# Kernel tuning notes

Measured on AMD Instinct MI355X. Metric: run time of the kernel, lower is better.

Reference implementation:

```python
import jax, jax.numpy as jnp
import numpy as np
import math

B, S, H, NH, R = 1, 1024, 4096, 32, 16
HD = H // NH
BLOCK = 64
PRUNE_RATIO = 0.5
NF4_TABLE = jnp.array([
    -1.0, -0.6961928009986877, -0.5250730514526367, -0.39491748809814453,
    -0.28444138169288635, -0.18477343022823334, -0.09105003625154495, 0.0,
    0.07958029955625534, 0.16093020141124725, 0.24611230194568634,
    0.33791524171829224, 0.4407098591327667, 0.5626170039176941,
    0.7229568362236023, 1.0], dtype=jnp.float32)


def dequant_nf4(codes, absmax):
    # codes: [out,in] int4 values in [0,16); absmax: per-64-elem block scale
    vals = NF4_TABLE[codes.reshape(-1)]                 # [out*in]
    vals = vals.reshape(-1, BLOCK) * absmax[:, None]    # blockwise rescale
    return vals.reshape(codes.shape)                    # [out,in]


def setup_inputs() -> dict:
    key = jax.random.key(0)
    ks = jax.random.split(key, 32)
    d = {"x": jax.random.normal(ks[0], (B, S, H), dtype=jnp.float32)}
    i = 1
    for n in ("q", "k", "v", "o"):
        d[f"w_{n}_codes"] = jax.random.randint(ks[i], (H, H), 0, 16, dtype=jnp.int32); i += 1
        d[f"w_{n}_absmax"] = jax.random.uniform(ks[i], (H * H // BLOCK,), dtype=jnp.float32) * 0.06; i += 1
        d[f"b_{n}"] = jax.random.normal(ks[i], (H,), dtype=jnp.float32) * 0.01; i += 1
        d[f"w_{n}_lora_a"] = jax.random.normal(ks[i], (H, R), dtype=jnp.float32) * (1.0 / math.sqrt(H)); i += 1
        d[f"w_{n}_lora_b"] = jax.random.normal(ks[i], (R, H), dtype=jnp.float32) * 0.02; i += 1
    causal = jnp.tril(jnp.ones((S, S), dtype=bool))
    d["attention_mask"] = jnp.where(causal, 0.0, -1e9).astype(jnp.float32)[None, None]
    return d


def _proj(x, codes, absmax, b, la, lb):
    w = dequant_nf4(codes, absmax).T          # [in,out]
    main = x @ w + b
    lora_a = x @ la                            # [B,S,R]
    return main + lora_a @ lb, main, lora_a


def _kth_val(t, use_abs=True):
    flat = jnp.abs(t).ravel() if use_abs else t.ravel()
    k = int(t.size * PRUNE_RATIO)
    return jnp.sort(flat)[k - 1]


def reference(x, w_q_codes, w_q_absmax, b_q, w_q_lora_a, w_q_lora_b,
              w_k_codes, w_k_absmax, b_k, w_k_lora_a, w_k_lora_b,
              w_v_codes, w_v_absmax, b_v, w_v_lora_a, w_v_lora_b,
              w_o_codes, w_o_absmax, b_o, w_o_lora_a, w_o_lora_b,
              attention_mask):
    q, _, _ = _proj(x, w_q_codes, w_q_absmax, b_q, w_q_lora_a, w_q_lora_b)
    k, _, _ = _proj(x, w_k_codes, w_k_absmax, b_k, w_k_lora_a, w_k_lora_b)
    v, _, _ = _proj(x, w_v_codes, w_v_absmax, b_v, w_v_lora_a, w_v_lora_b)
    # [B,S,H] -> [B,NH,S,HD]
    qh = q.reshape(B, S, NH, HD).transpose(0, 2, 1, 3)
    kh = k.reshape(B, S, NH, HD).transpose(0, 2, 1, 3)
    vh = v.reshape(B, S, NH, HD).transpose(0, 2, 1, 3)
    s = jnp.einsum("bhqd,bhkd->bhqk", qh, kh) / math.sqrt(HD) + attention_mask
    a = jax.nn.softmax(s, axis=-1)
    o = jnp.einsum("bhqk,bhkd->bhqd", a, vh)
    o = o.transpose(0, 2, 1, 3).reshape(B, S, H)
    o_final, _, _ = _proj(o, w_o_codes, w_o_absmax, b_o, w_o_lora_a, w_o_lora_b)
    # iteration < 10 branch: magnitude-pruning thresholds via kth smallest value
    kth_vals = jnp.stack([
        _kth_val(x), _kth_val(qh), _kth_val(kh), _kth_val(vh),
        _kth_val(a, use_abs=False), _kth_val(o)])
    return o_final, kth_vals
```

## Files before the change

### kernel.cpp

```cpp
#include <hip/hip_runtime.h>

#define S_LEN  1024
#define H_DIM  4096
#define NHEAD  32
#define HEAD_D 128
#define RANK   16
#define KE3    4160
#define KEO    4160
#define TOTP   ((long)NHEAD * S_LEN * S_LEN)

typedef __bf16 bf16x8 __attribute__((ext_vector_type(8)));
typedef float  f32x4  __attribute__((ext_vector_type(4)));
typedef unsigned short ushort8v __attribute__((ext_vector_type(8)));

#define GLOAD_LDS16(g, l) __builtin_amdgcn_global_load_lds( \
    (const __attribute__((address_space(1))) unsigned int*)(g), \
    (__attribute__((address_space(3))) unsigned int*)(l), 16, 0, 0)

__device__ const float NF4_TAB[16] = {
    -1.0f, -0.6961928009986877f, -0.5250730514526367f, -0.39491748809814453f,
    -0.28444138169288635f, -0.18477343022823334f, -0.09105003625154495f, 0.0f,
    0.07958029955625534f, 0.16093020141124725f, 0.24611230194568634f,
    0.33791524171829224f, 0.4407098591327667f, 0.5626170039176941f,
    0.7229568362236023f, 1.0f};

__device__ __forceinline__ unsigned short f2bf(float f) {
    unsigned int u = __builtin_bit_cast(unsigned int, f);
    u = (u + 0x7FFFu + ((u >> 16) & 1u)) >> 16;
    return (unsigned short)u;
}

__device__ __forceinline__ float bf2f(unsigned short s) {
    return __builtin_bit_cast(float, (unsigned int)s << 16);
}

__device__ __forceinline__ void dequant_body(
    const int* __restrict__ codes, const float* __restrict__ absmax,
    unsigned short* __restrict__ out, long i, int ostride) {
    int4 c0 = *(const int4*)(codes + i);
    int4 c1 = *(const int4*)(codes + i + 4);
    float am = absmax[i >> 6];
    long orow = i >> 12;
    int  col  = (int)(i & 4095);
    ushort8v r;
    r[0] = f2bf(NF4_TAB[c0.x] * am);
    r[1] = f2bf(NF4_TAB[c0.y] * am);
    r[2] = f2bf(NF4_TAB[c0.z] * am);
    r[3] = f2bf(NF4_TAB[c0.w] * am);
    r[4] = f2bf(NF4_TAB[c1.x] * am);
    r[5] = f2bf(NF4_TAB[c1.y] * am);
    r[6] = f2bf(NF4_TAB[c1.z] * am);
    r[7] = f2bf(NF4_TAB[c1.w] * am);
    *(ushort8v*)(out + orow * ostride + col) = r;
}

__global__ __launch_bounds__(256) void xcast_lora(
    const float* __restrict__ x, const float* __restrict__ la0,
    const float* __restrict__ la1, const float* __restrict__ la2,
    unsigned short* __restrict__ xb_ext) {
    __shared__ float xs[4096];
    int m = (int)blockIdx.x;
    int tid = threadIdx.x;
    const float* xr = x + (long)m * H_DIM;
    int c = tid * 16;
    float4 f0 = *(const float4*)(xr + c);
    float4 f1 = *(const float4*)(xr + c + 4);
    float4 f2 = *(const float4*)(xr + c + 8);
    float4 f3 = *(const float4*)(xr + c + 12);
    *(float4*)(xs + c)      = f0;
    *(float4*)(xs + c + 4)  = f1;
    *(float4*)(xs + c + 8)  = f2;
    *(float4*)(xs + c + 12) = f3;
    ushort8v r0, r1;
    r0[0] = f2bf(f0.x); r0[1] = f2bf(f0.y); r0[2] = f2bf(f0.z); r0[3] = f2bf(f0.w);
    r0[4] = f2bf(f1.x); r0[5] = f2bf(f1.y); r0[6] = f2bf(f1.z); r0[7] = f2bf(f1.w);
    r1[0] = f2bf(f2.x); r1[1] = f2bf(f2.y); r1[2] = f2bf(f2.z); r1[3] = f2bf(f2.w);
    r1[4] = f2bf(f3.x); r1[5] = f2bf(f3.y); r1[6] = f2bf(f3.z); r1[7] = f2bf(f3.w);
    unsigned short* orow = xb_ext + (long)m * KE3 + c;
    *(ushort8v*)orow = r0;
    *(ushort8v*)(orow + 8) = r1;
    __syncthreads();
    int w = tid >> 6, lane = tid & 63;
    if (w < 3) {
        const float* la = (w == 0) ? la0 : (w == 1) ? la1 : la2;
        float s[16];
#pragma unroll
        for (int r = 0; r < 16; ++r) s[r] = 0.f;
        for (int k = lane; k < H_DIM; k += 64) {
            float xv = xs[k];
            const float4* lr = (const float4*)(la + (long)k * RANK);
            float4 q0 = lr[0], q1 = lr[1], q2 = lr[2], q3 = lr[3];
            s[0] += xv * q0.x;  s[1] += xv * q0.y;  s[2] += xv * q0.z;  s[3] += xv * q0.w;
            s[4] += xv * q1.x;  s[5] += xv * q1.y;  s[6] += xv * q1.z;  s[7] += xv * q1.w;
            s[8] += xv * q2.x;  s[9] += xv * q2.y;  s[10] += xv * q2.z; s[11] += xv * q2.w;
            s[12] += xv * q3.x; s[13] += xv * q3.y; s[14] += xv * q3.z; s[15] += xv * q3.w;
        }
        for (int off = 32; off; off >>= 1)
#pragma unroll
            for (int r = 0; r < 16; ++r) s[r] += __shfl_xor(s[r], off);
        if (lane == 0)
#pragma unroll
            for (int r = 0; r < 16; ++r)
                xb_ext[(long)m * KE3 + 4096 + 16 * w + r] = f2bf(s[r]);
    } else if (lane < 16) {
        xb_ext[(long)m * KE3 + 4144 + lane] = 0;
    }
}

__global__ __launch_bounds__(256) void prep_weights(
    const int* __restrict__ c0, const int* __restrict__ c1,
    const int* __restrict__ c2, const int* __restrict__ c3,
    const float* __restrict__ a0, const float* __restrict__ a1,
    const float* __restrict__ a2, const float* __restrict__ a3,
    const float* __restrict__ lb0, const float* __restrict__ lb1,
    const float* __restrict__ lb2, const float* __restrict__ lb3,
    const float* __restrict__ b0, const float* __restrict__ b1,
    const float* __restrict__ b2,
    unsigned short* __restrict__ wqkv, unsigned short* __restrict__ wo,
    float* __restrict__ bias3, unsigned int* __restrict__ hist, long n) {
    int p = blockIdx.y;
    long bx = blockIdx.x;
    int tid = threadIdx.x;
    if (bx < 8192) {
        const int* codes = (p == 0) ? c0 : (p == 1) ? c1 : (p == 2) ? c2 : c3;
        const float* am  = (p == 0) ? a0 : (p == 1) ? a1 : (p == 2) ? a2 : a3;
        long i = (bx * 256 + tid) * 8;
        if (i >= n) return;
        if (p < 3) dequant_body(codes, am, wqkv + (size_t)p * H_DIM * KE3, i, KE3);
        else       dequant_body(codes, am, wo, i, KEO);
        return;
    }
    if (bx < 9216) {
        long g = (bx - 8192) * 256 + tid;
        int row = (int)(g >> 6), c = (int)(g & 63);
        if (p < 3) {
            const float* lb = (p == 0) ? lb0 : (p == 1) ? lb1 : lb2;
            unsigned int r = (unsigned int)(c - 16 * p);
            float v = (r < 16u) ? lb[r * H_DIM + row] : 0.f;
            wqkv[(size_t)p * H_DIM * KE3 + (long)row * KE3 + 4096 + c] = f2bf(v);
            if (g < H_DIM) {
                const float* bp = (p == 0) ? b0 : (p == 1) ? b1 : b2;
                bias3[(size_t)p * H_DIM + g] = bp[g];
            }
            return;
        }
        float v = (c < 16) ? lb3[c * H_DIM + row] : 0.f;
        wo[(long)row * KEO + 4096 + c] = f2bf(v);
        return;
    }
    if (p == 1) {
        long g = (bx - 9216) * 256 + tid;
        if (g < 6 * 16384) hist[g] = 0u;
    }
}

__global__ __launch_bounds__(256) void lora_ao_kernel(
    unsigned short* __restrict__ ob_ext, const float* __restrict__ la) {
    int m = blockIdx.x;
    const unsigned short* xr = ob_ext + (long)m * KEO;
    int tid = threadIdx.x, lane = tid & 63, wid = tid >> 6;
    float s[4] = {0.f, 0.f, 0.f, 0.f};
    for (int k0 = lane * 8; k0 < H_DIM; k0 += 512) {
        ushort8v xv8 = *(const ushort8v*)(xr + k0);
#pragma unroll
        for (int j = 0; j < 8; ++j) {
            float xv = bf2f(xv8[j]);
            float4 q = *(const float4*)(la + (long)(k0 + j) * RANK + wid * 4);
            s[0] += xv * q.x; s[1] += xv * q.y;
            s[2] += xv * q.z; s[3] += xv * q.w;
        }
    }
    for (int off = 32; off; off >>= 1)
        for (int r = 0; r < 4; ++r) s[r] += __shfl_down(s[r], off);
    if (lane == 0) {
        for (int r = 0; r < 4; ++r)
            ob_ext[(long)m * KEO + 4096 + wid * 4 + r] = f2bf(s[r]);
        for (int r = 0; r < 12; ++r)
            ob_ext[(long)m * KEO + 4112 + wid * 12 + r] = 0;
    }
}

template<int MODE>
__global__ __launch_bounds__(256) void gemm_nt(
    const unsigned short* __restrict__ A, const unsigned short* __restrict__ B,
    void* __restrict__ Cv, void* __restrict__ Cv2, const float* __restrict__ bias,
    int K, int lda, int ldb, int ldc,
    long strideA, long strideB, long strideC, float alpha,
    const unsigned short* __restrict__ tsrc, unsigned short* __restrict__ tdst) {
    __shared__ unsigned short As[128][64];
    __shared__ unsigned short Bs[128][64];
    const int tid = threadIdx.x;
    int bm, bn;
    int k0s = 0, k0e = K;
    if (MODE == 1) {
        int i = blockIdx.x;
        if (i >= 36) {
            unsigned short (*tl)[33] = (unsigned short(*)[33])&As[0][0];
            int tb = (i - 36) + 4 * blockIdx.z;
            int tx = tid & 31, ty = tid >> 5;
            for (int tile = tb; tile < 4096; tile += 128) {
                int tc = tile & 127, ts = tile >> 7;
                int c0 = tc * 32, s0 = ts * 32;
                for (int j = 0; j < 32; j += 8)
                    tl[ty + j][tx] = tsrc[(long)(s0 + ty + j) * H_DIM + c0 + tx];
                __syncthreads();
                for (int j = 0; j < 32; j += 8)
                    tdst[(long)(c0 + ty + j) * S_LEN + s0 + tx] = tl[tx][ty + j];
                __syncthreads();
            }
            return;
        }
        int tm = (int)((sqrtf(8.f * i + 1.f) - 1.f) * 0.5f);
        if ((tm + 1) * (tm + 2) / 2 <= i) tm++;
        if (tm * (tm + 1) / 2 > i) tm--;
        int tn = i - tm * (tm + 1) / 2;
        bm = tm * 128; bn = tn * 128;
    } else {
        bm = blockIdx.y * 128; bn = blockIdx.x * 128;
        if (MODE == 2) { int kl = bm + 128; if (kl < k0e) k0e = kl; }
    }
    const unsigned short* Ab = A;
    const unsigned short* Bb = B;
    long coff = 0;
    void* Cuse = Cv;
    if (MODE == 3) {
        int Kh = (K / 2) & ~63;
        k0s = blockIdx.z ? Kh : 0;
        k0e = blockIdx.z ? K : Kh;
        Cuse = blockIdx.z ? Cv2 : Cv;
    } else {
        Ab += (long)blockIdx.z * strideA;
        Bb += (long)blockIdx.z * strideB;
        coff = (long)blockIdx.z * strideC;
    }
    const int lane = tid & 63, wid = tid >> 6;
    const int wm = (wid >> 1) * 64, wn = (wid & 1) * 64;
    const int srow = lane >> 3;
    const int scol = ((lane & 7) ^ srow) << 3;
    const int r0 = wid * 8 + srow;
    const unsigned short* gA0 = Ab + (long)(bm + r0) * lda + scol;
    const unsigned short* gB0 = Bb + (long)(bn + r0) * ldb + scol;
    f32x4 acc[4][4] = {};
    const int q = lane >> 4, rr = lane & 15;
    const int colh0 = ((q ^ (rr & 7)) << 3);
    const int colh1 = colh0 ^ 32;
    for (int k0 = k0s; k0 < k0e; k0 += 64) {
#pragma unroll
        for (int p = 0; p < 4; ++p) {
            GLOAD_LDS16(gA0 + (long)p * 32 * lda + k0, &As[p * 32 + wid * 8][0]);
            GLOAD_LDS16(gB0 + (long)p * 32 * ldb + k0, &Bs[p * 32 + wid * 8][0]);
        }
        __syncthreads();
        bf16x8 af[4], bfr[4];
#pragma unroll
        for (int i = 0; i < 4; ++i) {
            af[i]  = __builtin_bit_cast(bf16x8, *(const uint4*)&As[wm + i * 16 + rr][colh0]);
            bfr[i] = __builtin_bit_cast(bf16x8, *(const uint4*)&Bs[wn + i * 16 + rr][colh0]);
        }
#pragma unroll
        for (int i = 0; i < 4; ++i)
#pragma unroll
            for (int j = 0; j < 4; ++j)
                acc[i][j] = __builtin_amdgcn_mfma_f32_16x16x32_bf16(
                    af[i], bfr[j], acc[i][j], 0, 0, 0);
#pragma unroll
        for (int i = 0; i < 4; ++i) {
            af[i]  = __builtin_bit_cast(bf16x8, *(const uint4*)&As[wm + i * 16 + rr][colh1]);
            bfr[i] = __builtin_bit_cast(bf16x8, *(const uint4*)&Bs[wn + i * 16 + rr][colh1]);
        }
#pragma unroll
        for (int i = 0; i < 4; ++i)
#pragma unroll
            for (int j = 0; j < 4; ++j)
                acc[i][j] = __builtin_amdgcn_mfma_f32_16x16x32_bf16(
                    af[i], bfr[j], acc[i][j], 0, 0, 0);
        __syncthreads();
    }
    const int cr = (lane >> 4) * 4;
    const int cc = lane & 15;
    float bv[4];
#pragma unroll
    for (int j = 0; j < 4; ++j)
        bv[j] = bias ? bias[(long)blockIdx.z * H_DIM + bn + wn + j * 16 + cc] : 0.f;
    if (MODE != 3) {
        unsigned short* Cb = (unsigned short*)Cuse + coff;
        for (int i = 0; i < 4; ++i)
            for (int j = 0; j < 4; ++j) {
                unsigned short* cp = Cb + (long)(bm + wm + i * 16 + cr) * ldc
                                        + (bn + wn + j * 16 + cc);
                for (int r = 0; r < 4; ++r)
                    cp[(long)r * ldc] = f2bf(acc[i][j][r] * alpha + bv[j]);
            }
    } else {
        float* Cb = (float*)Cuse + coff;
        for (int i = 0; i < 4; ++i)
            for (int j = 0; j < 4; ++j) {
                float* cp = Cb + (long)(bm + wm + i * 16 + cr) * ldc
                               + (bn + wn + j * 16 + cc);
                for (int r = 0; r < 4; ++r)
                    cp[(long)r * ldc] = acc[i][j][r] * alpha + bv[j];
            }
    }
}

__global__ __launch_bounds__(256) void softmax_causal(unsigned short* __restrict__ scores16) {
    int b = blockIdx.x;
    int h = b >> 9, pr = b & 511;
    int tid = threadIdx.x, lane = tid & 63, wid = tid >> 6;
    __shared__ float red[4], red2[4];
    for (int half = 0; half < 2; ++half) {
        int i = half ? (S_LEN - 1 - pr) : pr;
        unsigned short* row = scores16 + ((long)h * S_LEN + i) * S_LEN;
        int L = i + 1;
        float v[4];
        float mx = -1e30f;
        for (int t = 0; t < 4; ++t) {
            int j = tid + (t << 8);
            v[t] = (j < L) ? bf2f(row[j]) : -1e30f;
            mx = fmaxf(mx, v[t]);
        }
        for (int off = 32; off; off >>= 1) mx = fmaxf(mx, __shfl_xor(mx, off));
        if (lane == 0) red[wid] = mx;
        __syncthreads();
        mx = fmaxf(fmaxf(red[0], red[1]), fmaxf(red[2], red[3]));
        float e[4], sum = 0.f;
        for (int t = 0; t < 4; ++t) {
            int j = tid + (t << 8);
            e[t] = (j < L) ? __expf(v[t] - mx) : 0.f;
            sum += e[t];
        }
        for (int off = 32; off; off >>= 1) sum += __shfl_xor(sum, off);
        if (lane == 0) red2[wid] = sum;
        __syncthreads();
        sum = red2[0] + red2[1] + red2[2] + red2[3];
        float inv = 1.f / sum;
        for (int t = 0; t < 4; ++t) {
            int j = tid + (t << 8);
            row[j] = f2bf(e[t] * inv);
        }
        __syncthreads();
    }
}

__global__ __launch_bounds__(256, 2) void hist6(
    const float* __restrict__ x, const unsigned short* __restrict__ qkv,
    const unsigned short* __restrict__ ob, const unsigned short* __restrict__ P,
    unsigned int* __restrict__ hist) {
    __shared__ unsigned int lh[16384];
    const long SH = (long)S_LEN * H_DIM;
    int t = threadIdx.x;
    int b = blockIdx.x;
    int ten, b0, nblk;
    if (b < 256)      { ten = 0; b0 = 0;   nblk = 256; }
    else if (b < 384) { ten = 1; b0 = 256; nblk = 128; }
    else if (b < 512) { ten = 2; b0 = 384; nblk = 128; }
    else if (b < 640) { ten = 3; b0 = 512; nblk = 128; }
    else if (b < 768) { ten = 4; b0 = 640; nblk = 128; }
    else              { ten = 5; b0 = 768; nblk = 768; }
    unsigned int* gh = hist + (long)ten * 16384;
    for (int k = t; k < 16384; k += 256) lh[k] = 0u;
    __syncthreads();
    long i = (long)(b - b0) * 256 + t;
    long stride = (long)nblk * 256;
    if (ten == 0) {
        for (; i < SH / 4; i += stride) {
            float4 v = *(const float4*)(x + i * 4);
            unsigned int u0 = (__builtin_bit_cast(unsigned int, v.x) & 0x7FFFFFFFu) >> 16;
            unsigned int u1 = (__builtin_bit_cast(unsigned int, v.y) & 0x7FFFFFFFu) >> 16;
            unsigned int u2 = (__builtin_bit_cast(unsigned int, v.z) & 0x7FFFFFFFu) >> 16;
            unsigned int u3 = (__builtin_bit_cast(unsigned int, v.w) & 0x7FFFFFFFu) >> 16;
            atomicAdd(&lh[u0 < 16384u ? u0 : 16383u], 1u);
            atomicAdd(&lh[u1 < 16384u ? u1 : 16383u], 1u);
            atomicAdd(&lh[u2 < 16384u ? u2 : 16383u], 1u);
            atomicAdd(&lh[u3 < 16384u ? u3 : 16383u], 1u);
        }
    } else if (ten <= 3) {
        const unsigned short* src = qkv + (size_t)(ten - 1) * SH;
        for (; i < SH / 8; i += stride) {
            ushort8v v = ((const ushort8v*)src)[i];
#pragma unroll
            for (int j = 0; j < 8; ++j) {
                unsigned int u = v[j] & 0x7FFFu;
                atomicAdd(&lh[u < 16384u ? u : 16383u], 1u);
            }
        }
    } else if (ten == 4) {
        for (; i < SH / 8; i += stride) {
            long off = (i >> 9) * KEO + ((i & 511) << 3);
            ushort8v v = *(const ushort8v*)(ob + off);
#pragma unroll
            for (int j = 0; j < 8; ++j) {
                unsigned int u = v[j] & 0x7FFFu;
                atomicAdd(&lh[u < 16384u ? u : 16383u], 1u);
            }
        }
    } else {
        unsigned int zc = 0;
        for (; i < TOTP / 8; i += stride) {
            ushort8v v = ((const ushort8v*)P)[i];
#pragma unroll
            for (int j = 0; j < 8; ++j) {
                unsigned int bb = v[j];
                if (bb == 0) zc++;
                else atomicAdd(&lh[bb < 16384u ? bb : 16383u], 1u);
            }
        }
        if (zc) atomicAdd(&lh[0], zc);
    }
    __syncthreads();
    for (int k = t; k < 16384; k += 256) {
        unsigned int c = lh[k];
        if (c) atomicAdd(&gh[k], c);
    }
}

__global__ __launch_bounds__(256) void finish_kernel(
    float* __restrict__ out, const float* __restrict__ part,
    const float* __restrict__ bias, const unsigned int* __restrict__ hist,
    float* __restrict__ out_kth) {
    int b = blockIdx.x;
    int t = threadIdx.x;
    if (b < 4096) {
        long idx = ((long)b * 256 + t) * 4;
        int n = (int)(idx & 4095);
        float4 o = *(float4*)(out + idx);
        float4 p = *(const float4*)(part + idx);
        float4 bb = *(const float4*)(bias + n);
        o.x += p.x + bb.x; o.y += p.y + bb.y; o.z += p.z + bb.z; o.w += p.w + bb.w;
        *(float4*)(out + idx) = o;
        return;
    }
    int ten = b - 4096;
    const unsigned int* h = hist + (long)ten * 16384;
    __shared__ unsigned int partl[256];
    unsigned int s = 0;
    for (int bb = 0; bb < 64; ++bb) s += h[t * 64 + bb];
    partl[t] = s;
    __syncthreads();
    if (t == 0) {
        long k = (ten == 5) ? TOTP / 2 : (long)S_LEN * H_DIM / 2;
        long c = 0;
        int ch = 0;
        for (; ch < 256; ++ch) {
            if (c + (long)partl[ch] >= k) break;
            c += partl[ch];
        }
        int bin = ch * 64;
        for (;; ++bin) {
            unsigned int hv = h[bin];
            if (c + (long)hv >= k) break;
            c += hv;
        }
        int slot = (ten == 4) ? 5 : (ten == 5) ? 4 : ten;
        out_kth[slot] = __builtin_bit_cast(float, (unsigned int)bin << 16);
    }
}

extern "C" void kernel_launch(void* const* d_in, const int* in_sizes, int n_in,
                              void* d_out, int out_size, void* d_ws, size_t ws_size,
                              hipStream_t stream) {
    (void)in_sizes; (void)n_in; (void)out_size; (void)ws_size;
    const float* x = (const float*)d_in[0];
    const int*   wcodes[4] = {(const int*)d_in[1], (const int*)d_in[6],
                              (const int*)d_in[11], (const int*)d_in[16]};
    const float* wabs[4]   = {(const float*)d_in[2], (const float*)d_in[7],
                              (const float*)d_in[12], (const float*)d_in[17]};
    const float* bias[4]   = {(const float*)d_in[3], (const float*)d_in[8],
                              (const float*)d_in[13], (const float*)d_in[18]};
    const float* lA[4]     = {(const float*)d_in[4], (const float*)d_in[9],
                              (const float*)d_in[14], (const float*)d_in[19]};
    const float* lB[4]     = {(const float*)d_in[5], (const float*)d_in[10],
                              (const float*)d_in[15], (const float*)d_in[20]};

    char* wp = (char*)d_ws;
    auto alloc = [&](size_t bytes) {
        char* p = wp; wp += (bytes + 255) & ~(size_t)255; return p;
    };
    const size_t SH  = (size_t)S_LEN * H_DIM;
    const long   nW  = (long)H_DIM * H_DIM;
    unsigned short* xb_ext = (unsigned short*)alloc((size_t)S_LEN * KE3 * 2);
    unsigned short* qkvb   = (unsigned short*)alloc(3 * SH * 2);
    unsigned short* vT     = (unsigned short*)alloc(SH * 2);
    unsigned short* ob_ext = (unsigned short*)alloc((size_t)S_LEN * KEO * 2);
    unsigned short* Wd_ext = (unsigned short*)alloc((size_t)H_DIM * KEO * 2);
    float*        opart  = (float*)alloc(SH * 4);
    float*        bias3  = (float*)alloc(3 * H_DIM * 4);
    unsigned int* hist   = (unsigned int*)alloc(6 * 16384 * 4);
    char* bigbuf = alloc((size_t)3 * H_DIM * KE3 * 2);
    unsigned short* Wqkv_ext = (unsigned short*)bigbuf;
    unsigned short* scores16 = (unsigned short*)bigbuf;

    float* out_final = (float*)d_out;
    float* out_kth   = out_final + SH;

    unsigned short* qb = qkvb;
    unsigned short* kb = qkvb + SH;
    unsigned short* vb = qkvb + 2 * SH;

    xcast_lora<<<S_LEN, 256, 0, stream>>>(x, lA[0], lA[1], lA[2], xb_ext);

    prep_weights<<<dim3(9600, 4), 256, 0, stream>>>(
        wcodes[0], wcodes[1], wcodes[2], wcodes[3],
        wabs[0], wabs[1], wabs[2], wabs[3],
        lB[0], lB[1], lB[2], lB[3],
        bias[0], bias[1], bias[2],
        Wqkv_ext, Wd_ext, bias3, hist, nW);

    gemm_nt<0><<<dim3(32, 8, 3), 256, 0, stream>>>(
        xb_ext, Wqkv_ext, qkvb, nullptr, bias3, KE3, KE3, KE3, H_DIM,
        0, (long)H_DIM * KE3, (long)SH, 1.0f, nullptr, nullptr);

    gemm_nt<1><<<dim3(40, 1, NHEAD), 256, 0, stream>>>(
        qb, kb, scores16, nullptr, nullptr, HEAD_D, H_DIM, H_DIM, S_LEN,
        128, 128, (long)S_LEN * S_LEN, 0.08838834764831845f, vb, vT);

    softmax_causal<<<NHEAD * S_LEN / 2, 256, 0, stream>>>(scores16);

    gemm_nt<2><<<dim3(1, 8, NHEAD), 256, 0, stream>>>(
        scores16, vT, ob_ext, nullptr, nullptr, S_LEN,
        S_LEN, S_LEN, KEO,
        (long)S_LEN * S_LEN, (long)HEAD_D * S_LEN, 128, 1.0f, nullptr, nullptr);

    lora_ao_kernel<<<S_LEN, 256, 0, stream>>>(ob_ext, lA[3]);

    gemm_nt<3><<<dim3(32, 8, 2), 256, 0, stream>>>(
        ob_ext, Wd_ext, out_final, opart, nullptr, KEO, KEO, KEO, H_DIM,
        0, 0, 0, 1.0f, nullptr, nullptr);

    hist6<<<1536, 256, 0, stream>>>(x, qkvb, ob_ext, scores16, hist);

    finish_kernel<<<4102, 256, 0, stream>>>(out_final, opart, bias[3], hist, out_kth);
}
```

Measured before the change: 722.5 us.

## Overlap O-projection weight dequant with QKV GEMM via extra blocks

The O-projection NF4 dequantization moves out of prep_weights into 192 extra blocks of the QKV GEMM launch, so it runs alongside the GEMM tiles instead of before them. The O LoRA-B padding columns are now written by xcast_lora. The GEMM template becomes a device body wrapped by per-mode kernels with constant arguments. This shortens the serial prep phase, at the cost of the dequant blocks competing with GEMM tiles for CUs and memory bandwidth.

```diff
diff --git a/kernel.cpp b/kernel.cpp
--- a/kernel.cpp
+++ b/kernel.cpp
@@ -57,10 +57,17 @@
 __global__ __launch_bounds__(256) void xcast_lora(
     const float* __restrict__ x, const float* __restrict__ la0,
     const float* __restrict__ la1, const float* __restrict__ la2,
-    unsigned short* __restrict__ xb_ext) {
+    const float* __restrict__ lb3,
+    unsigned short* __restrict__ xb_ext, unsigned short* __restrict__ wo) {
     __shared__ float xs[4096];
     int m = (int)blockIdx.x;
     int tid = threadIdx.x;
+    {
+        long g = (long)m * 256 + tid;
+        int row = (int)(g >> 6), c = (int)(g & 63);
+        float v = (c < 16) ? lb3[c * H_DIM + row] : 0.f;
+        wo[(long)row * KEO + 4096 + c] = f2bf(v);
+    }
     const float* xr = x + (long)m * H_DIM;
     int c = tid * 16;
     float4 f0 = *(const float4*)(xr + c);
@@ -109,43 +116,37 @@
 
 __global__ __launch_bounds__(256) void prep_weights(
     const int* __restrict__ c0, const int* __restrict__ c1,
-    const int* __restrict__ c2, const int* __restrict__ c3,
+    const int* __restrict__ c2,
     const float* __restrict__ a0, const float* __restrict__ a1,
-    const float* __restrict__ a2, const float* __restrict__ a3,
+    const float* __restrict__ a2,
     const float* __restrict__ lb0, const float* __restrict__ lb1,
-    const float* __restrict__ lb2, const float* __restrict__ lb3,
+    const float* __restrict__ lb2,
     const float* __restrict__ b0, const float* __restrict__ b1,
     const float* __restrict__ b2,
-    unsigned short* __restrict__ wqkv, unsigned short* __restrict__ wo,
+    unsigned short* __restrict__ wqkv,
     float* __restrict__ bias3, unsigned int* __restrict__ hist, long n) {
     int p = blockIdx.y;
     long bx = blockIdx.x;
     int tid = threadIdx.x;
     if (bx < 8192) {
-        const int* codes = (p == 0) ? c0 : (p == 1) ? c1 : (p == 2) ? c2 : c3;
-        const float* am  = (p == 0) ? a0 : (p == 1) ? a1 : (p == 2) ? a2 : a3;
+        const int* codes = (p == 0) ? c0 : (p == 1) ? c1 : c2;
+        const float* am  = (p == 0) ? a0 : (p == 1) ? a1 : a2;
         long i = (bx * 256 + tid) * 8;
         if (i >= n) return;
-        if (p < 3) dequant_body(codes, am, wqkv + (size_t)p * H_DIM * KE3, i, KE3);
-        else       dequant_body(codes, am, wo, i, KEO);
+        dequant_body(codes, am, wqkv + (size_t)p * H_DIM * KE3, i, KE3);
         return;
     }
     if (bx < 9216) {
         long g = (bx - 8192) * 256 + tid;
         int row = (int)(g >> 6), c = (int)(g & 63);
-        if (p < 3) {
-            const float* lb = (p == 0) ? lb0 : (p == 1) ? lb1 : lb2;
-            unsigned int r = (unsigned int)(c - 16 * p);
-            float v = (r < 16u) ? lb[r * H_DIM + row] : 0.f;
-            wqkv[(size_t)p * H_DIM * KE3 + (long)row * KE3 + 4096 + c] = f2bf(v);
-            if (g < H_DIM) {
-                const float* bp = (p == 0) ? b0 : (p == 1) ? b1 : b2;
-                bias3[(size_t)p * H_DIM + g] = bp[g];
-            }
-            return;
-        }
-        float v = (c < 16) ? lb3[c * H_DIM + row] : 0.f;
-        wo[(long)row * KEO + 4096 + c] = f2bf(v);
+        const float* lb = (p == 0) ? lb0 : (p == 1) ? lb1 : lb2;
+        unsigned int r = (unsigned int)(c - 16 * p);
+        float v = (r < 16u) ? lb[r * H_DIM + row] : 0.f;
+        wqkv[(size_t)p * H_DIM * KE3 + (long)row * KE3 + 4096 + c] = f2bf(v);
+        if (g < H_DIM) {
+            const float* bp = (p == 0) ? b0 : (p == 1) ? b1 : b2;
+            bias3[(size_t)p * H_DIM + g] = bp[g];
+        }
         return;
     }
     if (p == 1) {
@@ -181,7 +182,7 @@
 }
 
 template<int MODE>
-__global__ __launch_bounds__(256) void gemm_nt(
+__device__ __forceinline__ void gemm_body(
     const unsigned short* __restrict__ A, const unsigned short* __restrict__ B,
     void* __restrict__ Cv, void* __restrict__ Cv2, const float* __restrict__ bias,
     int K, int lda, int ldb, int ldc,
@@ -301,6 +302,45 @@
                     cp[(long)r * ldc] = acc[i][j][r] * alpha + bv[j];
             }
     }
+}
+
+__global__ __launch_bounds__(256) void gemm_qkv(
+    const unsigned short* __restrict__ A, const unsigned short* __restrict__ B,
+    void* __restrict__ Cv, const float* __restrict__ bias,
+    const int* __restrict__ c3, const float* __restrict__ a3,
+    unsigned short* __restrict__ wo, long nw) {
+    if (blockIdx.x >= 32) {
+        int r = (int)(blockIdx.x - 32) + 8 * (int)(blockIdx.y + 8 * blockIdx.z);
+        int tid = threadIdx.x;
+        for (long i = ((long)r * 256 + tid) * 8; i < nw; i += 192L * 256 * 8)
+            dequant_body(c3, a3, wo, i, KEO);
+        return;
+    }
+    gemm_body<0>(A, B, Cv, nullptr, bias, KE3, KE3, KE3, H_DIM,
+                 0, (long)H_DIM * KE3, (long)S_LEN * H_DIM, 1.0f, nullptr, nullptr);
+}
+
+__global__ __launch_bounds__(256) void gemm_scores(
+    const unsigned short* __restrict__ A, const unsigned short* __restrict__ B,
+    void* __restrict__ Cv, const unsigned short* __restrict__ tsrc,
+    unsigned short* __restrict__ tdst) {
+    gemm_body<1>(A, B, Cv, nullptr, nullptr, HEAD_D, H_DIM, H_DIM, S_LEN,
+                 128, 128, (long)S_LEN * S_LEN, 0.08838834764831845f, tsrc, tdst);
+}
+
+__global__ __launch_bounds__(256) void gemm_pv(
+    const unsigned short* __restrict__ A, const unsigned short* __restrict__ B,
+    void* __restrict__ Cv) {
+    gemm_body<2>(A, B, Cv, nullptr, nullptr, S_LEN, S_LEN, S_LEN, KEO,
+                 (long)S_LEN * S_LEN, (long)HEAD_D * S_LEN, 128, 1.0f,
+                 nullptr, nullptr);
+}
+
+__global__ __launch_bounds__(256) void gemm_oproj(
+    const unsigned short* __restrict__ A, const unsigned short* __restrict__ B,
+    void* __restrict__ Cv, void* __restrict__ Cv2) {
+    gemm_body<3>(A, B, Cv, Cv2, nullptr, KEO, KEO, KEO, H_DIM,
+                 0, 0, 0, 1.0f, nullptr, nullptr);
 }
 
 __global__ __launch_bounds__(256) void softmax_causal(unsigned short* __restrict__ scores16) {
@@ -497,35 +537,30 @@
     unsigned short* kb = qkvb + SH;
     unsigned short* vb = qkvb + 2 * SH;
 
-    xcast_lora<<<S_LEN, 256, 0, stream>>>(x, lA[0], lA[1], lA[2], xb_ext);
-
-    prep_weights<<<dim3(9600, 4), 256, 0, stream>>>(
-        wcodes[0], wcodes[1], wcodes[2], wcodes[3],
-        wabs[0], wabs[1], wabs[2], wabs[3],
-        lB[0], lB[1], lB[2], lB[3],
+    xcast_lora<<<S_LEN, 256, 0, stream>>>(x, lA[0], lA[1], lA[2], lB[3],
+                                          xb_ext, Wd_ext);
+
+    prep_weights<<<dim3(9600, 3), 256, 0, stream>>>(
+        wcodes[0], wcodes[1], wcodes[2],
+        wabs[0], wabs[1], wabs[2],
+        lB[0], lB[1], lB[2],
         bias[0], bias[1], bias[2],
-        Wqkv_ext, Wd_ext, bias3, hist, nW);
-
-    gemm_nt<0><<<dim3(32, 8, 3), 256, 0, stream>>>(
-        xb_ext, Wqkv_ext, qkvb, nullptr, bias3, KE3, KE3, KE3, H_DIM,
-        0, (long)H_DIM * KE3, (long)SH, 1.0f, nullptr, nullptr);
-
-    gemm_nt<1><<<dim3(40, 1, NHEAD), 256, 0, stream>>>(
-        qb, kb, scores16, nullptr, nullptr, HEAD_D, H_DIM, H_DIM, S_LEN,
-        128, 128, (long)S_LEN * S_LEN, 0.08838834764831845f, vb, vT);
+        Wqkv_ext, bias3, hist, nW);
+
+    gemm_qkv<<<dim3(40, 8, 3), 256, 0, stream>>>(
+        xb_ext, Wqkv_ext, qkvb, bias3, wcodes[3], wabs[3], Wd_ext, nW);
+
+    gemm_scores<<<dim3(40, 1, NHEAD), 256, 0, stream>>>(
+        qb, kb, scores16, vb, vT);
 
     softmax_causal<<<NHEAD * S_LEN / 2, 256, 0, stream>>>(scores16);
 
-    gemm_nt<2><<<dim3(1, 8, NHEAD), 256, 0, stream>>>(
-        scores16, vT, ob_ext, nullptr, nullptr, S_LEN,
-        S_LEN, S_LEN, KEO,
-        (long)S_LEN * S_LEN, (long)HEAD_D * S_LEN, 128, 1.0f, nullptr, nullptr);
+    gemm_pv<<<dim3(1, 8, NHEAD), 256, 0, stream>>>(scores16, vT, ob_ext);
 
     lora_ao_kernel<<<S_LEN, 256, 0, stream>>>(ob_ext, lA[3]);
 
-    gemm_nt<3><<<dim3(32, 8, 2), 256, 0, stream>>>(
-        ob_ext, Wd_ext, out_final, opart, nullptr, KEO, KEO, KEO, H_DIM,
-        0, 0, 0, 1.0f, nullptr, nullptr);
+    gemm_oproj<<<dim3(32, 8, 2), 256, 0, stream>>>(
+        ob_ext, Wd_ext, out_final, opart);
 
     hist6<<<1536, 256, 0, stream>>>(x, qkvb, ob_ext, scores16, hist);
 
```

Result: slower. 770.1 us (+6.6%).
